# Performance work log

Hardware: AMD Instinct MI355X
Metric: run time of the kernel (lower is better)

## Reference

```python
import jax, jax.numpy as jnp
import numpy as np

B, N, RESC, LAT, UNIT = 8, 32, 256.0, 1536, 512
CHS = [64, 64, 128, 256, 512, 512]
HS = [128, 64, 32, 16, 8, 1]


def _align(feat, P):
    # torch F.grid_sample(feat, 2*P.unsqueeze(-2)/RESC - 1, 'bilinear', 'border', align_corners=False).squeeze(-1)
    # feat: [B,C,H,W], P: [B,M,2] (x,y) pixel coords in [0,RESC); returns [B,C,M]
    Bn, C, H, W = feat.shape
    gx = 2.0 * P[..., 0] / RESC - 1.0
    gy = 2.0 * P[..., 1] / RESC - 1.0
    # align_corners=False unnormalize, then border clamp
    x = jnp.clip(((gx + 1.0) * W - 1.0) * 0.5, 0.0, W - 1.0)
    y = jnp.clip(((gy + 1.0) * H - 1.0) * 0.5, 0.0, H - 1.0)
    x0 = jnp.floor(x); y0 = jnp.floor(y)
    wx = (x - x0)[:, None, :]; wy = (y - y0)[:, None, :]
    x0i = x0.astype(jnp.int32); y0i = y0.astype(jnp.int32)
    x1i = jnp.minimum(x0i + 1, W - 1); y1i = jnp.minimum(y0i + 1, H - 1)
    flat = feat.reshape(Bn, C, H * W)
    def gat(yi, xi):
        return jnp.take_along_axis(flat, (yi * W + xi)[:, None, :], axis=2)  # [B,C,M]
    v00 = gat(y0i, x0i); v01 = gat(y0i, x1i); v10 = gat(y1i, x0i); v11 = gat(y1i, x1i)
    return v00 * (1 - wx) * (1 - wy) + v01 * wx * (1 - wy) + v10 * (1 - wx) * wy + v11 * wx * wy


def _conv1(x, w, b):
    # 1x1 Conv1d: [B,Cin,M] x [Cout,Cin] -> [B,Cout,M]
    return jnp.einsum('bci,oc->boi', x, w) + b[None, :, None]


def _rescls(x, p):
    # ResCls(n=1): intro -> (relu(BN) -> chorus, residual) -> outro ; BN in eval mode
    iw, ib, bg, bb, bm, bv, cw, cb, ow, ob = p
    x = _conv1(x, iw, ib)
    d = jax.nn.relu((x - bm[None, :, None]) * (bg / jnp.sqrt(bv + 1e-5))[None, :, None] + bb[None, :, None])
    x = x + _conv1(d, cw, cb)
    return _conv1(x, ow, ob)


def _forward(feats, P, n, gp, pp):
    # node features: concat of per-level aligned features  [B, LAT, N]
    F_ = jnp.concatenate([_align(f, P) for f in feats], axis=1)
    # edge midpoints ep[b, i*N+j] = (P[i] + P[j]) / 2  -> [B, N*N, 2]
    ep = ((P[:, :, None, :] + P[:, None, :, :]) * 0.5).reshape(B, N * N, 2)
    # L: first LAT channels = F[:, :, i], next LAT channels = F[:, :, j]
    Fi = jnp.broadcast_to(F_[:, :, :, None], (B, LAT, N, N)).reshape(B, LAT, N * N)
    Fj = jnp.broadcast_to(F_[:, :, None, :], (B, LAT, N, N)).reshape(B, LAT, N * N)
    E = jnp.concatenate([_align(f, ep) for f in feats], axis=1)  # [B, LAT, N*N]
    CE = jnp.concatenate([Fi, Fj, E], axis=1)  # [B, 3*LAT, N*N]
    gate = jax.nn.sigmoid(_rescls(CE, gp))  # [B, 1, N*N]
    pr = _rescls(CE, pp)  # [B, 64, N*N]
    pr = pr / jnp.maximum(jnp.linalg.norm(pr, axis=1, keepdims=True), 1e-12)  # F.normalize(dim=1)
    m = jnp.arange(N) < n[:, None]  # [B, N]
    mask = (m[:, None, :] & m[:, :, None]).reshape(B, 1, N * N).astype(CE.dtype)
    return (gate * pr * mask).reshape(B, 64, N, N)


def setup_inputs() -> dict:
    key = jax.random.key(0)
    ks = jax.random.split(key, 20)
    d = {}
    for i, (c, h) in enumerate(zip(CHS, HS)):
        d[f'feat{i}'] = jax.random.normal(ks[i], (B, c, h, h), jnp.float32)
    d['P'] = jax.random.uniform(ks[6], (B, N, 2), jnp.float32) * RESC
    d['n'] = jax.random.randint(ks[7], (B,), 16, N + 1, jnp.int32)
    def w(k, shape):
        return jax.random.normal(k, shape, jnp.float32) * 0.02
    for pre, cout, k0 in (('g', 1, 8), ('p', 64, 12)):
        d[pre + '_iw'] = w(ks[k0], (UNIT, 3 * LAT)); d[pre + '_ib'] = jnp.zeros((UNIT,), jnp.float32)
        d[pre + '_bg'] = jnp.ones((UNIT,), jnp.float32); d[pre + '_bb'] = jnp.zeros((UNIT,), jnp.float32)
        d[pre + '_bm'] = jnp.zeros((UNIT,), jnp.float32)
        d[pre + '_bv'] = jax.random.uniform(ks[k0 + 1], (UNIT,), jnp.float32) + 0.5
        d[pre + '_cw'] = w(ks[k0 + 2], (UNIT, UNIT)); d[pre + '_cb'] = jnp.zeros((UNIT,), jnp.float32)
        d[pre + '_ow'] = w(ks[k0 + 3], (cout, UNIT)); d[pre + '_ob'] = jnp.zeros((cout,), jnp.float32)
    return d


def reference(feat0, feat1, feat2, feat3, feat4, feat5, P, n,
              g_iw, g_ib, g_bg, g_bb, g_bm, g_bv, g_cw, g_cb, g_ow, g_ob,
              p_iw, p_ib, p_bg, p_bb, p_bm, p_bv, p_cw, p_cb, p_ow, p_ob):
    feats = (feat0, feat1, feat2, feat3, feat4, feat5)
    gp = (g_iw, g_ib, g_bg, g_bb, g_bm, g_bv, g_cw, g_cb, g_ow, g_ob)
    pp = (p_iw, p_ib, p_bg, p_bb, p_bm, p_bv, p_cw, p_cb, p_ow, p_ob)
    return _forward(feats, P, n, gp, pp)
```

## Files before the change

kernel.cpp:

```cpp
#include <hip/hip_runtime.h>
#include <hip/hip_bf16.h>

using bf16 = __hip_bfloat16;
using short8 = __attribute__((ext_vector_type(8))) short;
using f32x4  = __attribute__((ext_vector_type(4))) float;
typedef unsigned int u32;

#define LAT_ 1536

__device__ __forceinline__ void glds16(const bf16* g, bf16* l) {
  __builtin_amdgcn_global_load_lds(
      (const __attribute__((address_space(1))) void*)g,
      (__attribute__((address_space(3))) void*)l, 16, 0, 0);
}
__device__ __forceinline__ float b2f(bf16 x) { return __bfloat162float(x); }
__device__ __forceinline__ bf16 f2b(float x) { return __float2bfloat16(x); }

template<int C, int W>
__device__ __forceinline__ void trans_tile(const float* __restrict__ src, bf16* __restrict__ dst,
                                           int b, int hw0, int c0, bf16 (*tile)[72], int t) {
  constexpr int HW = W * W;
  {
    int cl = t >> 2, h0 = (t & 3) * 16;
    const float* sp = src + (long)(b * C + c0 + cl) * HW + hw0 + h0;
    #pragma unroll
    for (int k = 0; k < 16; k += 4) {
      float4 v = *(const float4*)(sp + k);
      tile[h0 + k + 0][cl] = f2b(v.x);
      tile[h0 + k + 1][cl] = f2b(v.y);
      tile[h0 + k + 2][cl] = f2b(v.z);
      tile[h0 + k + 3][cl] = f2b(v.w);
    }
  }
  __syncthreads();
  {
    int hwl = t >> 2, cc = (t & 3) * 16;
    bf16* dp = dst + ((long)b * HW + hw0 + hwl) * C + c0 + cc;
    #pragma unroll
    for (int k = 0; k < 16; k += 2) {
      __hip_bfloat162 pr;
      pr.x = tile[hwl][cc + k];
      pr.y = tile[hwl][cc + k + 1];
      *(__hip_bfloat162*)(dp + k) = pr;
    }
  }
}

__global__ __launch_bounds__(256) void prep_k(
    const float* __restrict__ g_iw, const float* __restrict__ p_iw,
    const float* __restrict__ p_cw, const float* __restrict__ p_ow, const float* __restrict__ f5,
    const float* __restrict__ g_bg, const float* __restrict__ g_bb, const float* __restrict__ g_bm,
    const float* __restrict__ g_bv, const float* __restrict__ p_bg, const float* __restrict__ p_bb,
    const float* __restrict__ p_bm, const float* __restrict__ p_bv,
    const float* __restrict__ g_ib, const float* __restrict__ p_ib, const float* __restrict__ p_cb,
    const float* __restrict__ g_ow, const float* __restrict__ g_cw,
    const float* __restrict__ g_cb, const float* __restrict__ g_ob,
    const float* __restrict__ f0, const float* __restrict__ f1, const float* __restrict__ f2,
    const float* __restrict__ f3, const float* __restrict__ f4,
    bf16* __restrict__ Wp, bf16* __restrict__ pcw16, bf16* __restrict__ pow16,
    bf16* __restrict__ T5, float* __restrict__ bnp, float* __restrict__ u,
    float* __restrict__ gacc, float* __restrict__ A4,
    bf16* __restrict__ T0, bf16* __restrict__ T1, bf16* __restrict__ T2,
    bf16* __restrict__ T3, bf16* __restrict__ T4) {
  __shared__ bf16 tile[64][72];
  __shared__ float red[256];
  int B = blockIdx.x, t = threadIdx.x;
  if (B < 18432) {
    int seg = B / 3072;
    int idx = (B % 3072) * 256 + t;
    if (idx < 512 * 1536) {
      int r = idx / 1536, c = idx % 1536;
      const float* src; int co;
      switch (seg) {
        case 0: src = g_iw; co = 0;    break;
        case 1: src = g_iw; co = 1536; break;
        case 2: src = p_iw; co = 0;    break;
        case 3: src = p_iw; co = 1536; break;
        case 4: src = g_iw; co = 3072; break;
        default: src = p_iw; co = 3072; break;
      }
      Wp[(long)seg * 512 * 1536 + idx] = f2b(src[(long)r * 4608 + co + c]);
    }
    return;
  }
  if (B < 19456) { int idx = (B - 18432) * 256 + t; pcw16[idx] = f2b(p_cw[idx]); return; }
  if (B < 19584) { int idx = (B - 19456) * 256 + t; pow16[idx] = f2b(p_ow[idx]); return; }
  if (B < 19600) { int idx = (B - 19584) * 256 + t; T5[idx] = f2b(f5[idx]); return; }
  if (B < 19602) {
    int k = (B - 19600) * 256 + t;
    if (k < 512) {
      float sg = g_bg[k] / sqrtf(g_bv[k] + 1e-5f);
      bnp[k] = sg; bnp[512 + k] = g_bb[k] - g_bm[k] * sg;
      float sp = p_bg[k] / sqrtf(p_bv[k] + 1e-5f);
      bnp[1024 + k] = sp; bnp[1536 + k] = p_bb[k] - p_bm[k] * sp;
      bnp[2048 + k] = g_ib[k]; bnp[2560 + k] = p_ib[k];
      bnp[3584 + k] = p_cb[k];
    }
    return;
  }
  if (B < 19610) {
    __shared__ float ured[4][64];
    int k0 = (B - 19602) * 64;
    int kk = t & 63, part = t >> 6;
    int k = k0 + kk;
    float s = 0.f;
    for (int o = part * 128; o < part * 128 + 128; ++o)
      s = fmaf(g_ow[o], g_cw[o * 512 + k], s);
    ured[part][kk] = s;
    __syncthreads();
    if (part == 0) u[k] = ured[0][kk] + ured[1][kk] + ured[2][kk] + ured[3][kk];
    return;
  }
  if (B == 19610) {
    red[t] = g_ow[t] * g_cb[t] + g_ow[t + 256] * g_cb[t + 256];
    __syncthreads();
    for (int off = 128; off; off >>= 1) {
      if (t < off) red[t] += red[t + off];
      __syncthreads();
    }
    if (t == 0) bnp[3072] = red[0] + g_ob[0];
    return;
  }
  if (B < 19643) { int idx = (B - 19611) * 256 + t; gacc[idx] = 0.f; return; }
  if (B >= 22651) { int idx = (B - 22651) * 256 + t; A4[idx] = 0.f; return; }
  {
    int q = B - 19643;
    int b = q / 376, tt = q % 376;
    if (tt < 256)      trans_tile<64, 128>(f0, T0, b, tt * 64, 0, tile, t);
    else if (tt < 320) trans_tile<64, 64 >(f1, T1, b, (tt - 256) * 64, 0, tile, t);
    else if (tt < 352) { int z = tt - 320; trans_tile<128, 32>(f2, T2, b, (z & 15) * 64, (z >> 4) * 64, tile, t); }
    else if (tt < 368) { int z = tt - 352; trans_tile<256, 16>(f3, T3, b, (z & 3) * 64, (z >> 2) * 64, tile, t); }
    else               { int z = tt - 368; trans_tile<512, 8 >(f4, T4, b, 0, z * 64, tile, t); }
  }
}

__device__ __forceinline__ float blo(u32 r) { return __uint_as_float(r << 16); }
__device__ __forceinline__ float bhi(u32 r) { return __uint_as_float(r & 0xffff0000u); }

template<int C, int W>
__device__ __forceinline__ void proc2(const bf16* __restrict__ T, int b,
    const float* MX, const float* MY, bf16* __restrict__ Sb, int koff, int t) {
  constexpr int C2 = C / 2, HW = W * W;
  const bf16* Tb = T + (long)b * HW * C;
  for (int idx = t; idx < 16 * C2; idx += 256) {
    int q = idx / C2, c2 = idx % C2;
    float x = MX[q], y = MY[q];
    float fx = fminf(fmaxf(x * ((float)W / 256.f) - 0.5f, 0.f), (float)(W - 1));
    float fy = fminf(fmaxf(y * ((float)W / 256.f) - 0.5f, 0.f), (float)(W - 1));
    float x0f = floorf(fx), y0f = floorf(fy);
    float wx = fx - x0f, wy = fy - y0f;
    int x0 = (int)x0f, y0 = (int)y0f;
    int x1 = min(x0 + 1, W - 1), y1 = min(y0 + 1, W - 1);
    u32 r00 = *(const u32*)&Tb[(y0 * W + x0) * C + 2 * c2];
    u32 r01 = *(const u32*)&Tb[(y0 * W + x1) * C + 2 * c2];
    u32 r10 = *(const u32*)&Tb[(y1 * W + x0) * C + 2 * c2];
    u32 r11 = *(const u32*)&Tb[(y1 * W + x1) * C + 2 * c2];
    float w00 = (1.f - wx) * (1.f - wy), w01 = wx * (1.f - wy);
    float w10 = (1.f - wx) * wy,        w11 = wx * wy;
    float vlo = blo(r00) * w00 + blo(r01) * w01 + blo(r10) * w10 + blo(r11) * w11;
    float vhi = bhi(r00) * w00 + bhi(r01) * w01 + bhi(r10) * w10 + bhi(r11) * w11;
    __hip_bfloat162 pr;
    pr.x = f2b(vlo); pr.y = f2b(vhi);
    *(__hip_bfloat162*)&Sb[(long)q * LAT_ + koff + 2 * c2] = pr;
  }
}

__global__ __launch_bounds__(256) void sample5_k(
    const bf16* __restrict__ T0, const bf16* __restrict__ T1, const bf16* __restrict__ T2,
    const bf16* __restrict__ T3, const bf16* __restrict__ T4, const bf16* __restrict__ T5,
    const float* __restrict__ P, bf16* __restrict__ Sball) {
  int b = blockIdx.z, p0 = blockIdx.x * 16, lvl = blockIdx.y, t = threadIdx.x;
  __shared__ float Px[32], Py[32], MX[16], MY[16];
  if (t < 32) { Px[t] = P[(b * 32 + t) * 2]; Py[t] = P[(b * 32 + t) * 2 + 1]; }
  __syncthreads();
  if (t < 16) {
    int m = p0 + t;
    float x, y;
    if (m < 32) { x = Px[m]; y = Py[m]; }
    else { int ij = m - 32, i = ij >> 5, j = ij & 31;
           x = 0.5f * (Px[i] + Px[j]); y = 0.5f * (Py[i] + Py[j]); }
    MX[t] = x; MY[t] = y;
  }
  __syncthreads();
  bf16* Sb = Sball + ((long)b * 1056 + p0) * LAT_;
  switch (lvl) {
    case 0: proc2<64, 128>(T0, b, MX, MY, Sb, 0,    t); break;
    case 1: proc2<64, 64 >(T1, b, MX, MY, Sb, 64,   t); break;
    case 2: proc2<128, 32>(T2, b, MX, MY, Sb, 128,  t); break;
    case 3: proc2<256, 16>(T3, b, MX, MY, Sb, 256,  t); break;
    case 4: proc2<512, 8 >(T4, b, MX, MY, Sb, 512,  t); break;
    default:
      for (int idx = t; idx < 16 * 256; idx += 256) {
        int q = idx >> 8, c2 = idx & 255;
        *(__hip_bfloat162*)&Sb[(long)q * LAT_ + 1024 + 2 * c2] =
            *(const __hip_bfloat162*)&T5[b * 512 + 2 * c2];
      }
  }
}

__global__ __launch_bounds__(256) void nodegemm_k(
    const bf16* __restrict__ Sball, const bf16* __restrict__ Wp, float* __restrict__ A4) {
  int b = blockIdx.z;
  int n0 = blockIdx.x * 64;
  int k0 = blockIdx.y * 384;
  int t = threadIdx.x, w = t >> 6, lane = t & 63;
  int nn = n0 + w * 16;
  int frow = lane & 15, fko = (lane >> 4) * 8;
  const bf16* Ab = Sball + (long)b * 1056 * LAT_;
  f32x4 acc[2] = {};
  for (int kb = k0; kb < k0 + 384; kb += 32) {
    short8 bq = *(const short8*)&Wp[(long)(nn + frow) * LAT_ + kb + fko];
    #pragma unroll
    for (int i = 0; i < 2; ++i) {
      short8 aq = *(const short8*)&Ab[(long)(i * 16 + frow) * LAT_ + kb + fko];
      acc[i] = __builtin_amdgcn_mfma_f32_16x16x32_bf16(aq, bq, acc[i], 0, 0, 0);
    }
  }
  #pragma unroll
  for (int i = 0; i < 2; ++i)
    #pragma unroll
    for (int r = 0; r < 4; ++r) {
      int m = i * 16 + (lane >> 4) * 4 + r;
      int n = nn + (lane & 15);
      atomicAdd(&A4[(long)b * 65536 + m * 2048 + n], acc[i][r]);
    }
}

__global__ __launch_bounds__(256) void edge_k(
    const bf16* __restrict__ Sball, const bf16* __restrict__ WpE,
    const float* __restrict__ bnp, const float* __restrict__ A4,
    const float* __restrict__ u, const float* __restrict__ g_ow,
    bf16* __restrict__ XFh, bf16* __restrict__ DH, float* __restrict__ gacc) {
  int b = blockIdx.z;
  int m0 = blockIdx.x * 128, n0 = blockIdx.y * 128;
  const bf16* A = Sball + (long)b * 1056 * LAT_ + 32 * LAT_;
  __shared__ bf16 Ash[2][128 * 64];
  __shared__ bf16 Bsh[2][128 * 64];
  int t = threadIdx.x, w = t >> 6, lane = t & 63;
  int mh = (w & 1) * 64, nh = (w >> 1) * 64;
  int frow = lane & 15, kq = lane >> 4;
  int srow = w * 8 + (lane >> 3), schunk = lane & 7;
  int rx7 = frow & 7;
  f32x4 acc[4][4] = {};

  auto STAGE = [&](int buf, int kt) {
    int kb = kt * 64;
    #pragma unroll
    for (int q = 0; q < 4; ++q) {
      int ra = q * 32 + srow;
      int sc = (schunk ^ (ra & 7)) * 8;
      glds16(&A[(long)(m0 + ra) * LAT_ + kb + sc],   &Ash[buf][ra * 64 + schunk * 8]);
      glds16(&WpE[(long)(n0 + ra) * LAT_ + kb + sc], &Bsh[buf][ra * 64 + schunk * 8]);
    }
  };

  STAGE(0, 0);
  STAGE(1, 1);
  asm volatile("s_waitcnt vmcnt(8)" ::: "memory");
  __builtin_amdgcn_sched_barrier(0);
  __builtin_amdgcn_s_barrier();
  #pragma unroll 1
  for (int kt = 0; kt < 24; ++kt) {
    int c = kt & 1;
    short8 af[2][4], bq[2][4];
    #pragma unroll
    for (int h = 0; h < 2; ++h) {
      int s8 = (((h * 4 + kq) ^ rx7) << 3);
      #pragma unroll
      for (int i = 0; i < 4; ++i)
        af[h][i] = *(const short8*)&Ash[c][(mh + i * 16 + frow) * 64 + s8];
      #pragma unroll
      for (int j = 0; j < 4; ++j)
        bq[h][j] = *(const short8*)&Bsh[c][(nh + j * 16 + frow) * 64 + s8];
    }
    asm volatile("s_waitcnt lgkmcnt(0)" ::: "memory");
    __builtin_amdgcn_sched_barrier(0);
    __builtin_amdgcn_s_barrier();
    if (kt + 2 < 24) STAGE(c, kt + 2);
    __builtin_amdgcn_sched_barrier(0);
    __builtin_amdgcn_s_setprio(1);
    #pragma unroll
    for (int h = 0; h < 2; ++h)
      #pragma unroll
      for (int i = 0; i < 4; ++i)
        #pragma unroll
        for (int j = 0; j < 4; ++j)
          acc[i][j] = __builtin_amdgcn_mfma_f32_16x16x32_bf16(af[h][i], bq[h][j], acc[i][j], 0, 0, 0);
    __builtin_amdgcn_s_setprio(0);
    if (kt < 23) {
      if (kt + 2 < 24) {
        asm volatile("s_waitcnt vmcnt(8)" ::: "memory");
      } else {
        asm volatile("s_waitcnt vmcnt(0)" ::: "memory");
      }
      __builtin_amdgcn_sched_barrier(0);
      __builtin_amdgcn_s_barrier();
    }
  }
  if (n0 < 512) {
    float pg[16];
    #pragma unroll
    for (int z = 0; z < 16; ++z) pg[z] = 0.f;
    #pragma unroll
    for (int i = 0; i < 4; ++i) {
      #pragma unroll
      for (int j = 0; j < 4; ++j) {
        int n = n0 + nh + j * 16 + (lane & 15);
        float gw = g_ow[n], uu = u[n];
        float sc2 = bnp[n], sh = bnp[512 + n], ib = bnp[2048 + n];
        #pragma unroll
        for (int r = 0; r < 4; ++r) {
          int m = m0 + mh + i * 16 + (lane >> 4) * 4 + r;
          float v = acc[i][j][r] + ib
                  + A4[((long)b * 32 + (m >> 5)) * 2048 + n]
                  + A4[((long)b * 32 + (m & 31)) * 2048 + 512 + n];
          float d = fmaxf(fmaf(v, sc2, sh), 0.f);
          pg[i * 4 + r] += gw * v + uu * d;
        }
      }
    }
    #pragma unroll
    for (int z = 0; z < 16; ++z) {
      float v = pg[z];
      v += __shfl_xor(v, 1, 16);
      v += __shfl_xor(v, 2, 16);
      v += __shfl_xor(v, 4, 16);
      v += __shfl_xor(v, 8, 16);
      pg[z] = v;
    }
    if ((lane & 15) == 0) {
      #pragma unroll
      for (int z = 0; z < 16; ++z) {
        int m = m0 + mh + (z >> 2) * 16 + (lane >> 4) * 4 + (z & 3);
        atomicAdd(&gacc[(long)b * 1024 + m], pg[z]);
      }
    }
  } else {
    #pragma unroll
    for (int i = 0; i < 4; ++i) {
      #pragma unroll
      for (int j = 0; j < 4; ++j) {
        int n = n0 + nh + j * 16 + (lane & 15);
        int np = n - 512;
        float sc2 = bnp[1024 + np], sh = bnp[1536 + np], ib = bnp[2048 + n];
        #pragma unroll
        for (int r = 0; r < 4; ++r) {
          int m = m0 + mh + i * 16 + (lane >> 4) * 4 + r;
          float v = acc[i][j][r] + ib
                  + A4[((long)b * 32 + (m >> 5)) * 2048 + 1024 + np]
                  + A4[((long)b * 32 + (m & 31)) * 2048 + 1536 + np];
          long e = ((long)b * 1024 + m) * 512 + np;
          XFh[e] = f2b(v);
          DH[e]  = f2b(fmaxf(fmaf(v, sc2, sh), 0.f));
        }
      }
    }
  }
}

__global__ __launch_bounds__(256) void chorus_k(
    const bf16* __restrict__ DH, const bf16* __restrict__ pcw16,
    const float* __restrict__ bnp, const bf16* __restrict__ XFh,
    bf16* __restrict__ Yp16) {
  int b = blockIdx.z;
  int m0 = blockIdx.x * 64, n0 = blockIdx.y * 128;
  const bf16* A = DH + (long)b * 1024 * 512;
  __shared__ bf16 Ash[64 * 64];
  __shared__ bf16 Bsh[128 * 64];
  int t = threadIdx.x, w = t >> 6, lane = t & 63;
  int nh = w * 32;
  int frow = lane & 15, kq = lane >> 4;
  int srow = t >> 3, schunk = t & 7;
  int rx7 = frow & 7;
  f32x4 acc[4][2] = {};
  for (int kb = 0; kb < 512; kb += 64) {
    #pragma unroll
    for (int q = 0; q < 2; ++q) {
      int ra = q * 32 + srow;
      int sc = (schunk ^ (ra & 7)) * 8;
      glds16(&A[(long)(m0 + ra) * 512 + kb + sc], &Ash[ra * 64 + schunk * 8]);
    }
    #pragma unroll
    for (int q = 0; q < 4; ++q) {
      int ra = q * 32 + srow;
      int sc = (schunk ^ (ra & 7)) * 8;
      glds16(&pcw16[(long)(n0 + ra) * 512 + kb + sc], &Bsh[ra * 64 + schunk * 8]);
    }
    __syncthreads();
    #pragma unroll
    for (int h = 0; h < 2; ++h) {
      int s8 = (((h * 4 + kq) ^ rx7) << 3);
      short8 af[4], bq[2];
      #pragma unroll
      for (int i = 0; i < 4; ++i)
        af[i] = *(const short8*)&Ash[(i * 16 + frow) * 64 + s8];
      #pragma unroll
      for (int j = 0; j < 2; ++j)
        bq[j] = *(const short8*)&Bsh[(nh + j * 16 + frow) * 64 + s8];
      #pragma unroll
      for (int i = 0; i < 4; ++i)
        #pragma unroll
        for (int j = 0; j < 2; ++j)
          acc[i][j] = __builtin_amdgcn_mfma_f32_16x16x32_bf16(af[i], bq[j], acc[i][j], 0, 0, 0);
    }
    __syncthreads();
  }
  #pragma unroll
  for (int i = 0; i < 4; ++i)
    #pragma unroll
    for (int j = 0; j < 2; ++j)
      #pragma unroll
      for (int r = 0; r < 4; ++r) {
        int m = m0 + i * 16 + (lane >> 4) * 4 + r;
        int n = n0 + nh + j * 16 + (lane & 15);
        float v = acc[i][j][r] + bnp[3584 + n]
                + b2f(XFh[((long)b * 1024 + m) * 512 + n]);
        Yp16[((long)b * 1024 + m) * 512 + n] = f2b(v);
      }
}

__global__ __launch_bounds__(256) void ofinal_k(
    const bf16* __restrict__ Yp16, const bf16* __restrict__ pow16,
    const float* __restrict__ p_ob, const float* __restrict__ gacc,
    const float* __restrict__ bnp, const int* __restrict__ nvec,
    float* __restrict__ out) {
  int b = blockIdx.y;
  int m0 = blockIdx.x * 32;
  const bf16* Ab = Yp16 + (long)b * 1024 * 512;
  __shared__ bf16 Ash[32][40];
  __shared__ bf16 Bsh[64][40];
  __shared__ float sred[2][2][16];
  __shared__ float ol[32][65];
  int t = threadIdx.x, w = t >> 6, lane = t & 63;
  int rowg = w & 1, colh = w >> 1;
  int mq = rowg * 16, cq = colh * 32;
  int frow = lane & 15, fko = (lane >> 4) * 8;
  f32x4 acc[2] = {};
  for (int kb = 0; kb < 512; kb += 32) {
    { int r = t >> 3, ko = (t & 7) * 4;
      *(uint2*)&Ash[r][ko] = *(const uint2*)&Ab[(long)(m0 + r) * 512 + kb + ko];
      int r2 = t >> 2, ko2 = (t & 3) * 8;
      *(uint4*)&Bsh[r2][ko2] = *(const uint4*)&pow16[(long)r2 * 512 + kb + ko2]; }
    __syncthreads();
    short8 af = *(const short8*)&Ash[mq + frow][fko];
    #pragma unroll
    for (int j = 0; j < 2; ++j) {
      short8 bq = *(const short8*)&Bsh[cq + j * 16 + frow][fko];
      acc[j] = __builtin_amdgcn_mfma_f32_16x16x32_bf16(af, bq, acc[j], 0, 0, 0);
    }
    __syncthreads();
  }
  float pr[2][4], ssl[4] = {0.f, 0.f, 0.f, 0.f};
  #pragma unroll
  for (int j = 0; j < 2; ++j) {
    float bias = p_ob[cq + j * 16 + (lane & 15)];
    #pragma unroll
    for (int r = 0; r < 4; ++r) {
      float v = acc[j][r] + bias;
      pr[j][r] = v;
      ssl[r] = fmaf(v, v, ssl[r]);
    }
  }
  #pragma unroll
  for (int r = 0; r < 4; ++r) {
    float v = ssl[r];
    v += __shfl_xor(v, 1, 16);
    v += __shfl_xor(v, 2, 16);
    v += __shfl_xor(v, 4, 16);
    v += __shfl_xor(v, 8, 16);
    ssl[r] = v;
  }
  if ((lane & 15) == 0) {
    #pragma unroll
    for (int r = 0; r < 4; ++r)
      sred[rowg][colh][(lane >> 4) * 4 + r] = ssl[r];
  }
  __syncthreads();
  int nb = nvec[b];
  float gconst = bnp[3072];
  float scale[4];
  #pragma unroll
  for (int r = 0; r < 4; ++r) {
    int row16 = (lane >> 4) * 4 + r;
    int m = m0 + mq + row16;
    float s2 = sred[rowg][0][row16] + sred[rowg][1][row16];
    float gl = gacc[(long)b * 1024 + m] + gconst;
    float gate = 1.f / (1.f + expf(-gl));
    int ii = m >> 5, jj = m & 31;
    float maskv = (ii < nb && jj < nb) ? 1.f : 0.f;
    scale[r] = gate * maskv / fmaxf(sqrtf(s2), 1e-12f);
  }
  #pragma unroll
  for (int j = 0; j < 2; ++j)
    #pragma unroll
    for (int r = 0; r < 4; ++r)
      ol[mq + (lane >> 4) * 4 + r][cq + j * 16 + (lane & 15)] = pr[j][r] * scale[r];
  __syncthreads();
  {
    int c = t >> 2, ms = (t & 3) * 8;
    float* op = out + ((long)b * 64 + c) * 1024 + m0 + ms;
    #pragma unroll
    for (int k = 0; k < 8; k += 4) {
      float4 v;
      v.x = ol[ms + k + 0][c];
      v.y = ol[ms + k + 1][c];
      v.z = ol[ms + k + 2][c];
      v.w = ol[ms + k + 3][c];
      *(float4*)(op + k) = v;
    }
  }
}

extern "C" void kernel_launch(void* const* d_in, const int* in_sizes, int n_in,
                              void* d_out, int out_size, void* d_ws, size_t ws_size,
                              hipStream_t stream) {
  const float* f0 = (const float*)d_in[0];
  const float* f1 = (const float*)d_in[1];
  const float* f2 = (const float*)d_in[2];
  const float* f3 = (const float*)d_in[3];
  const float* f4 = (const float*)d_in[4];
  const float* f5 = (const float*)d_in[5];
  const float* P  = (const float*)d_in[6];
  const int*   n  = (const int*)d_in[7];
  const float *g_iw=(const float*)d_in[8],  *g_ib=(const float*)d_in[9],
              *g_bg=(const float*)d_in[10], *g_bb=(const float*)d_in[11],
              *g_bm=(const float*)d_in[12], *g_bv=(const float*)d_in[13],
              *g_cw=(const float*)d_in[14], *g_cb=(const float*)d_in[15],
              *g_ow=(const float*)d_in[16], *g_ob=(const float*)d_in[17];
  const float *p_iw=(const float*)d_in[18], *p_ib=(const float*)d_in[19],
              *p_bg=(const float*)d_in[20], *p_bb=(const float*)d_in[21],
              *p_bm=(const float*)d_in[22], *p_bv=(const float*)d_in[23],
              *p_cw=(const float*)d_in[24], *p_cb=(const float*)d_in[25],
              *p_ow=(const float*)d_in[26], *p_ob=(const float*)d_in[27];
  float* out = (float*)d_out;
  char* wsb = (char*)d_ws;

  bf16*  Sb    = (bf16*)(wsb + 0);
  bf16*  Wp    = (bf16*)(wsb + 25952256);
  bf16*  pcw16 = (bf16*)(wsb + 35389440);
  bf16*  pow16 = (bf16*)(wsb + 35913728);
  bf16*  T5    = (bf16*)(wsb + 35979264);
  float* bnp   = (float*)(wsb + 35987456);
  float* u     = (float*)(wsb + 36003840);
  float* gacc  = (float*)(wsb + 36005888);
  float* A4    = (float*)(wsb + 36038656);
  bf16*  XFh   = (bf16*)(wsb + 38135808);
  bf16*  DH    = (bf16*)(wsb + 46524416);
  bf16*  Yp16  = (bf16*)(wsb + 54913024);
  bf16*  T0 = (bf16*)(wsb + 38135808);
  bf16*  T1 = (bf16*)(wsb + 54913024);
  bf16*  T2 = (bf16*)(wsb + 59107328);
  bf16*  T3 = (bf16*)(wsb + 61204480);
  bf16*  T4 = (bf16*)(wsb + 62253056);
  bf16*  WpE = Wp + (long)2048 * LAT_;

  prep_k<<<24699, 256, 0, stream>>>(g_iw, p_iw, p_cw, p_ow, f5,
      g_bg, g_bb, g_bm, g_bv, p_bg, p_bb, p_bm, p_bv, g_ib, p_ib, p_cb,
      g_ow, g_cw, g_cb, g_ob, f0, f1, f2, f3, f4,
      Wp, pcw16, pow16, T5, bnp, u, gacc, A4, T0, T1, T2, T3, T4);
  sample5_k<<<dim3(66, 6, 8), 256, 0, stream>>>(T0, T1, T2, T3, T4, T5, P, Sb);
  nodegemm_k<<<dim3(32, 4, 8), 256, 0, stream>>>(Sb, Wp, A4);
  edge_k<<<dim3(8, 8, 8), 256, 0, stream>>>(Sb, WpE, bnp, A4, u, g_ow, XFh, DH, gacc);
  chorus_k<<<dim3(16, 4, 8), 256, 0, stream>>>(DH, pcw16, bnp, XFh, Yp16);
  ofinal_k<<<dim3(32, 8), 256, 0, stream>>>(Yp16, pow16, p_ob, gacc, bnp, n, out);
}
```

Measured before the change: 242.7 us.

## Halve edge GEMM M-tile and replace double-buffered pipeline with single-buffer loop

The edge GEMM kernel now uses 64x128 tiles instead of 128x128, doubling the grid to 1024 blocks. The hand-scheduled double-buffered LDS pipeline (manual vmcnt waits, priority bumps, prefetch two stages ahead) is replaced by a simple single-buffer loop: load, __syncthreads, compute, __syncthreads. The aim is more blocks in flight for occupancy and latency hiding, at the cost of losing explicit load/compute overlap inside a block and doing more B-tile loads per output.

```diff
diff --git a/kernel.cpp b/kernel.cpp
--- a/kernel.cpp
+++ b/kernel.cpp
@@ -232,77 +232,54 @@
     const float* __restrict__ u, const float* __restrict__ g_ow,
     bf16* __restrict__ XFh, bf16* __restrict__ DH, float* __restrict__ gacc) {
   int b = blockIdx.z;
-  int m0 = blockIdx.x * 128, n0 = blockIdx.y * 128;
+  int m0 = blockIdx.x * 64, n0 = blockIdx.y * 128;
   const bf16* A = Sball + (long)b * 1056 * LAT_ + 32 * LAT_;
-  __shared__ bf16 Ash[2][128 * 64];
-  __shared__ bf16 Bsh[2][128 * 64];
+  __shared__ bf16 Ash[64 * 64];
+  __shared__ bf16 Bsh[128 * 64];
   int t = threadIdx.x, w = t >> 6, lane = t & 63;
-  int mh = (w & 1) * 64, nh = (w >> 1) * 64;
+  int mh = (w & 1) * 32, nh = (w >> 1) * 64;
   int frow = lane & 15, kq = lane >> 4;
-  int srow = w * 8 + (lane >> 3), schunk = lane & 7;
+  int srow = t >> 3, schunk = t & 7;
   int rx7 = frow & 7;
-  f32x4 acc[4][4] = {};
-
-  auto STAGE = [&](int buf, int kt) {
-    int kb = kt * 64;
-    #pragma unroll
-    for (int q = 0; q < 4; ++q) {
+  f32x4 acc[2][4] = {};
+  for (int kb = 0; kb < LAT_; kb += 64) {
+    #pragma unroll
+    for (int q = 0; q < 2; ++q) {
       int ra = q * 32 + srow;
       int sc = (schunk ^ (ra & 7)) * 8;
-      glds16(&A[(long)(m0 + ra) * LAT_ + kb + sc],   &Ash[buf][ra * 64 + schunk * 8]);
-      glds16(&WpE[(long)(n0 + ra) * LAT_ + kb + sc], &Bsh[buf][ra * 64 + schunk * 8]);
-    }
-  };
-
-  STAGE(0, 0);
-  STAGE(1, 1);
-  asm volatile("s_waitcnt vmcnt(8)" ::: "memory");
-  __builtin_amdgcn_sched_barrier(0);
-  __builtin_amdgcn_s_barrier();
-  #pragma unroll 1
-  for (int kt = 0; kt < 24; ++kt) {
-    int c = kt & 1;
-    short8 af[2][4], bq[2][4];
+      glds16(&A[(long)(m0 + ra) * LAT_ + kb + sc], &Ash[ra * 64 + schunk * 8]);
+    }
+    #pragma unroll
+    for (int q = 0; q < 4; ++q) {
+      int rb = q * 32 + srow;
+      int sc = (schunk ^ (rb & 7)) * 8;
+      glds16(&WpE[(long)(n0 + rb) * LAT_ + kb + sc], &Bsh[rb * 64 + schunk * 8]);
+    }
+    __syncthreads();
     #pragma unroll
     for (int h = 0; h < 2; ++h) {
       int s8 = (((h * 4 + kq) ^ rx7) << 3);
-      #pragma unroll
-      for (int i = 0; i < 4; ++i)
-        af[h][i] = *(const short8*)&Ash[c][(mh + i * 16 + frow) * 64 + s8];
+      short8 af[2], bq[4];
+      #pragma unroll
+      for (int i = 0; i < 2; ++i)
+        af[i] = *(const short8*)&Ash[(mh + i * 16 + frow) * 64 + s8];
       #pragma unroll
       for (int j = 0; j < 4; ++j)
-        bq[h][j] = *(const short8*)&Bsh[c][(nh + j * 16 + frow) * 64 + s8];
-    }
-    asm volatile("s_waitcnt lgkmcnt(0)" ::: "memory");
-    __builtin_amdgcn_sched_barrier(0);
-    __builtin_amdgcn_s_barrier();
-    if (kt + 2 < 24) STAGE(c, kt + 2);
-    __builtin_amdgcn_sched_barrier(0);
-    __builtin_amdgcn_s_setprio(1);
-    #pragma unroll
-    for (int h = 0; h < 2; ++h)
-      #pragma unroll
-      for (int i = 0; i < 4; ++i)
+        bq[j] = *(const short8*)&Bsh[(nh + j * 16 + frow) * 64 + s8];
+      #pragma unroll
+      for (int i = 0; i < 2; ++i)
         #pragma unroll
         for (int j = 0; j < 4; ++j)
-          acc[i][j] = __builtin_amdgcn_mfma_f32_16x16x32_bf16(af[h][i], bq[h][j], acc[i][j], 0, 0, 0);
-    __builtin_amdgcn_s_setprio(0);
-    if (kt < 23) {
-      if (kt + 2 < 24) {
-        asm volatile("s_waitcnt vmcnt(8)" ::: "memory");
-      } else {
-        asm volatile("s_waitcnt vmcnt(0)" ::: "memory");
-      }
-      __builtin_amdgcn_sched_barrier(0);
-      __builtin_amdgcn_s_barrier();
-    }
+          acc[i][j] = __builtin_amdgcn_mfma_f32_16x16x32_bf16(af[i], bq[j], acc[i][j], 0, 0, 0);
+    }
+    __syncthreads();
   }
   if (n0 < 512) {
-    float pg[16];
-    #pragma unroll
-    for (int z = 0; z < 16; ++z) pg[z] = 0.f;
-    #pragma unroll
-    for (int i = 0; i < 4; ++i) {
+    float pg[8];
+    #pragma unroll
+    for (int z = 0; z < 8; ++z) pg[z] = 0.f;
+    #pragma unroll
+    for (int i = 0; i < 2; ++i) {
       #pragma unroll
       for (int j = 0; j < 4; ++j) {
         int n = n0 + nh + j * 16 + (lane & 15);
@@ -320,7 +297,7 @@
       }
     }
     #pragma unroll
-    for (int z = 0; z < 16; ++z) {
+    for (int z = 0; z < 8; ++z) {
       float v = pg[z];
       v += __shfl_xor(v, 1, 16);
       v += __shfl_xor(v, 2, 16);
@@ -330,14 +307,14 @@
     }
     if ((lane & 15) == 0) {
       #pragma unroll
-      for (int z = 0; z < 16; ++z) {
+      for (int z = 0; z < 8; ++z) {
         int m = m0 + mh + (z >> 2) * 16 + (lane >> 4) * 4 + (z & 3);
         atomicAdd(&gacc[(long)b * 1024 + m], pg[z]);
       }
     }
   } else {
     #pragma unroll
-    for (int i = 0; i < 4; ++i) {
+    for (int i = 0; i < 2; ++i) {
       #pragma unroll
       for (int j = 0; j < 4; ++j) {
         int n = n0 + nh + j * 16 + (lane & 15);
@@ -560,7 +537,7 @@
       Wp, pcw16, pow16, T5, bnp, u, gacc, A4, T0, T1, T2, T3, T4);
   sample5_k<<<dim3(66, 6, 8), 256, 0, stream>>>(T0, T1, T2, T3, T4, T5, P, Sb);
   nodegemm_k<<<dim3(32, 4, 8), 256, 0, stream>>>(Sb, Wp, A4);
-  edge_k<<<dim3(8, 8, 8), 256, 0, stream>>>(Sb, WpE, bnp, A4, u, g_ow, XFh, DH, gacc);
+  edge_k<<<dim3(16, 8, 8), 256, 0, stream>>>(Sb, WpE, bnp, A4, u, g_ow, XFh, DH, gacc);
   chorus_k<<<dim3(16, 4, 8), 256, 0, stream>>>(DH, pcw16, bnp, XFh, Yp16);
   ofinal_k<<<dim3(32, 8), 256, 0, stream>>>(Yp16, pow16, p_ob, gacc, bnp, n, out);
 }
```

New measurement: 255.9 us. 5.5% more time.

## Fold chorus conv into outro weights, eliminating chorus GEMM kernel

Applied to the files above, without the earlier changes.

Because the outro is linear, p_ow·(x + p_cw·d + p_cb) is rewritten as [p_ow | p_ow·p_cw]·[x; d] plus a folded bias. The folded 64x1024 weight is precomputed in prep_k, and ofinal_k now runs K=1024 over XFh and DH directly. This drops the 512x512 chorus GEMM over 8192 rows and the Yp16 round trip. In exchange, ofinal does twice the K work, and prep spends naive serial dot products building the combined weight, with a small precision change from the bf16 folded weights.

```diff
diff --git a/kernel.cpp b/kernel.cpp
--- a/kernel.cpp
+++ b/kernel.cpp
@@ -53,11 +53,12 @@
     const float* __restrict__ g_bv, const float* __restrict__ p_bg, const float* __restrict__ p_bb,
     const float* __restrict__ p_bm, const float* __restrict__ p_bv,
     const float* __restrict__ g_ib, const float* __restrict__ p_ib, const float* __restrict__ p_cb,
+    const float* __restrict__ p_ob,
     const float* __restrict__ g_ow, const float* __restrict__ g_cw,
     const float* __restrict__ g_cb, const float* __restrict__ g_ob,
     const float* __restrict__ f0, const float* __restrict__ f1, const float* __restrict__ f2,
     const float* __restrict__ f3, const float* __restrict__ f4,
-    bf16* __restrict__ Wp, bf16* __restrict__ pcw16, bf16* __restrict__ pow16,
+    bf16* __restrict__ Wp, bf16* __restrict__ powW2,
     bf16* __restrict__ T5, float* __restrict__ bnp, float* __restrict__ u,
     float* __restrict__ gacc, float* __restrict__ A4,
     bf16* __restrict__ T0, bf16* __restrict__ T1, bf16* __restrict__ T2,
@@ -83,8 +84,31 @@
     }
     return;
   }
-  if (B < 19456) { int idx = (B - 18432) * 256 + t; pcw16[idx] = f2b(p_cw[idx]); return; }
-  if (B < 19584) { int idx = (B - 19456) * 256 + t; pow16[idx] = f2b(p_ow[idx]); return; }
+  if (B < 18560) {
+    int idx = (B - 18432) * 256 + t;
+    int o = idx >> 9, k = idx & 511;
+    powW2[(long)o * 1024 + k] = f2b(p_ow[o * 512 + k]);
+    return;
+  }
+  if (B < 18688) {
+    int idx = (B - 18560) * 256 + t;
+    int o = idx >> 9, ci = idx & 511;
+    float s = 0.f;
+    for (int co = 0; co < 512; ++co)
+      s = fmaf(p_ow[o * 512 + co], p_cw[co * 512 + ci], s);
+    powW2[(long)o * 1024 + 512 + ci] = f2b(s);
+    return;
+  }
+  if (B == 18688) {
+    if (t < 64) {
+      float s = 0.f;
+      for (int co = 0; co < 512; ++co)
+        s = fmaf(p_ow[t * 512 + co], p_cb[co], s);
+      bnp[3200 + t] = s + p_ob[t];
+    }
+    return;
+  }
+  if (B < 19584) return;
   if (B < 19600) { int idx = (B - 19584) * 256 + t; T5[idx] = f2b(f5[idx]); return; }
   if (B < 19602) {
     int k = (B - 19600) * 256 + t;
@@ -358,75 +382,15 @@
   }
 }
 
-__global__ __launch_bounds__(256) void chorus_k(
-    const bf16* __restrict__ DH, const bf16* __restrict__ pcw16,
-    const float* __restrict__ bnp, const bf16* __restrict__ XFh,
-    bf16* __restrict__ Yp16) {
-  int b = blockIdx.z;
-  int m0 = blockIdx.x * 64, n0 = blockIdx.y * 128;
-  const bf16* A = DH + (long)b * 1024 * 512;
-  __shared__ bf16 Ash[64 * 64];
-  __shared__ bf16 Bsh[128 * 64];
-  int t = threadIdx.x, w = t >> 6, lane = t & 63;
-  int nh = w * 32;
-  int frow = lane & 15, kq = lane >> 4;
-  int srow = t >> 3, schunk = t & 7;
-  int rx7 = frow & 7;
-  f32x4 acc[4][2] = {};
-  for (int kb = 0; kb < 512; kb += 64) {
-    #pragma unroll
-    for (int q = 0; q < 2; ++q) {
-      int ra = q * 32 + srow;
-      int sc = (schunk ^ (ra & 7)) * 8;
-      glds16(&A[(long)(m0 + ra) * 512 + kb + sc], &Ash[ra * 64 + schunk * 8]);
-    }
-    #pragma unroll
-    for (int q = 0; q < 4; ++q) {
-      int ra = q * 32 + srow;
-      int sc = (schunk ^ (ra & 7)) * 8;
-      glds16(&pcw16[(long)(n0 + ra) * 512 + kb + sc], &Bsh[ra * 64 + schunk * 8]);
-    }
-    __syncthreads();
-    #pragma unroll
-    for (int h = 0; h < 2; ++h) {
-      int s8 = (((h * 4 + kq) ^ rx7) << 3);
-      short8 af[4], bq[2];
-      #pragma unroll
-      for (int i = 0; i < 4; ++i)
-        af[i] = *(const short8*)&Ash[(i * 16 + frow) * 64 + s8];
-      #pragma unroll
-      for (int j = 0; j < 2; ++j)
-        bq[j] = *(const short8*)&Bsh[(nh + j * 16 + frow) * 64 + s8];
-      #pragma unroll
-      for (int i = 0; i < 4; ++i)
-        #pragma unroll
-        for (int j = 0; j < 2; ++j)
-          acc[i][j] = __builtin_amdgcn_mfma_f32_16x16x32_bf16(af[i], bq[j], acc[i][j], 0, 0, 0);
-    }
-    __syncthreads();
-  }
-  #pragma unroll
-  for (int i = 0; i < 4; ++i)
-    #pragma unroll
-    for (int j = 0; j < 2; ++j)
-      #pragma unroll
-      for (int r = 0; r < 4; ++r) {
-        int m = m0 + i * 16 + (lane >> 4) * 4 + r;
-        int n = n0 + nh + j * 16 + (lane & 15);
-        float v = acc[i][j][r] + bnp[3584 + n]
-                + b2f(XFh[((long)b * 1024 + m) * 512 + n]);
-        Yp16[((long)b * 1024 + m) * 512 + n] = f2b(v);
-      }
-}
-
 __global__ __launch_bounds__(256) void ofinal_k(
-    const bf16* __restrict__ Yp16, const bf16* __restrict__ pow16,
-    const float* __restrict__ p_ob, const float* __restrict__ gacc,
+    const bf16* __restrict__ XFh, const bf16* __restrict__ DH,
+    const bf16* __restrict__ powW2, const float* __restrict__ gacc,
     const float* __restrict__ bnp, const int* __restrict__ nvec,
     float* __restrict__ out) {
   int b = blockIdx.y;
   int m0 = blockIdx.x * 32;
-  const bf16* Ab = Yp16 + (long)b * 1024 * 512;
+  const bf16* AX = XFh + (long)b * 1024 * 512;
+  const bf16* AD = DH  + (long)b * 1024 * 512;
   __shared__ bf16 Ash[32][40];
   __shared__ bf16 Bsh[64][40];
   __shared__ float sred[2][2][16];
@@ -436,11 +400,13 @@
   int mq = rowg * 16, cq = colh * 32;
   int frow = lane & 15, fko = (lane >> 4) * 8;
   f32x4 acc[2] = {};
-  for (int kb = 0; kb < 512; kb += 32) {
+  #pragma unroll 1
+  for (int kb = 0; kb < 1024; kb += 32) {
+    const bf16* Asrc = (kb < 512) ? (AX + kb) : (AD + (kb - 512));
     { int r = t >> 3, ko = (t & 7) * 4;
-      *(uint2*)&Ash[r][ko] = *(const uint2*)&Ab[(long)(m0 + r) * 512 + kb + ko];
+      *(uint2*)&Ash[r][ko] = *(const uint2*)&Asrc[(long)(m0 + r) * 512 + ko];
       int r2 = t >> 2, ko2 = (t & 3) * 8;
-      *(uint4*)&Bsh[r2][ko2] = *(const uint4*)&pow16[(long)r2 * 512 + kb + ko2]; }
+      *(uint4*)&Bsh[r2][ko2] = *(const uint4*)&powW2[(long)r2 * 1024 + kb + ko2]; }
     __syncthreads();
     short8 af = *(const short8*)&Ash[mq + frow][fko];
     #pragma unroll
@@ -453,7 +419,7 @@
   float pr[2][4], ssl[4] = {0.f, 0.f, 0.f, 0.f};
   #pragma unroll
   for (int j = 0; j < 2; ++j) {
-    float bias = p_ob[cq + j * 16 + (lane & 15)];
+    float bias = bnp[3200 + cq + j * 16 + (lane & 15)];
     #pragma unroll
     for (int r = 0; r < 4; ++r) {
       float v = acc[j][r] + bias;
@@ -537,8 +503,6 @@
 
   bf16*  Sb    = (bf16*)(wsb + 0);
   bf16*  Wp    = (bf16*)(wsb + 25952256);
-  bf16*  pcw16 = (bf16*)(wsb + 35389440);
-  bf16*  pow16 = (bf16*)(wsb + 35913728);
   bf16*  T5    = (bf16*)(wsb + 35979264);
   float* bnp   = (float*)(wsb + 35987456);
   float* u     = (float*)(wsb + 36003840);
@@ -546,21 +510,20 @@
   float* A4    = (float*)(wsb + 36038656);
   bf16*  XFh   = (bf16*)(wsb + 38135808);
   bf16*  DH    = (bf16*)(wsb + 46524416);
-  bf16*  Yp16  = (bf16*)(wsb + 54913024);
   bf16*  T0 = (bf16*)(wsb + 38135808);
   bf16*  T1 = (bf16*)(wsb + 54913024);
   bf16*  T2 = (bf16*)(wsb + 59107328);
   bf16*  T3 = (bf16*)(wsb + 61204480);
   bf16*  T4 = (bf16*)(wsb + 62253056);
+  bf16*  powW2 = (bf16*)(wsb + 62777344);
   bf16*  WpE = Wp + (long)2048 * LAT_;
 
   prep_k<<<24699, 256, 0, stream>>>(g_iw, p_iw, p_cw, p_ow, f5,
-      g_bg, g_bb, g_bm, g_bv, p_bg, p_bb, p_bm, p_bv, g_ib, p_ib, p_cb,
+      g_bg, g_bb, g_bm, g_bv, p_bg, p_bb, p_bm, p_bv, g_ib, p_ib, p_cb, p_ob,
       g_ow, g_cw, g_cb, g_ob, f0, f1, f2, f3, f4,
-      Wp, pcw16, pow16, T5, bnp, u, gacc, A4, T0, T1, T2, T3, T4);
+      Wp, powW2, T5, bnp, u, gacc, A4, T0, T1, T2, T3, T4);
   sample5_k<<<dim3(66, 6, 8), 256, 0, stream>>>(T0, T1, T2, T3, T4, T5, P, Sb);
   nodegemm_k<<<dim3(32, 4, 8), 256, 0, stream>>>(Sb, Wp, A4);
   edge_k<<<dim3(8, 8, 8), 256, 0, stream>>>(Sb, WpE, bnp, A4, u, g_ow, XFh, DH, gacc);
-  chorus_k<<<dim3(16, 4, 8), 256, 0, stream>>>(DH, pcw16, bnp, XFh, Yp16);
-  ofinal_k<<<dim3(32, 8), 256, 0, stream>>>(Yp16, pow16, p_ob, gacc, bnp, n, out);
-}
+  ofinal_k<<<dim3(32, 8), 256, 0, stream>>>(XFh, DH, powW2, gacc, bnp, n, out);
+}
```

Result: slower. 258.0 us (+6.3%).
